# Kernel tuning notes

Hardware: AMD Instinct MI355X
Metric: run time of the kernel (lower is better)

## Reference

```python
import jax, jax.numpy as jnp
import numpy as np

HEADS = 16
D_MODEL = 1024
D_K = D_MODEL // HEADS


def setup_inputs() -> dict:
    key = jax.random.key(0)
    ks = jax.random.split(key, 11)
    B, S = 4, 2048
    scale = 1.0 / np.sqrt(D_MODEL)
    inp = {
        "query": jax.random.normal(ks[0], (B, S, D_MODEL), dtype=jnp.float32),
        "key": jax.random.normal(ks[1], (B, S, D_MODEL), dtype=jnp.float32),
        "value": jax.random.normal(ks[2], (B, S, D_MODEL), dtype=jnp.float32),
        "Wq": jax.random.normal(ks[3], (D_MODEL, D_MODEL), dtype=jnp.float32) * scale,
        "bq": jnp.zeros((D_MODEL,), dtype=jnp.float32),
        "Wk": jax.random.normal(ks[4], (D_MODEL, D_MODEL), dtype=jnp.float32) * scale,
        "bk": jnp.zeros((D_MODEL,), dtype=jnp.float32),
        "Wv": jax.random.normal(ks[5], (D_MODEL, D_MODEL), dtype=jnp.float32) * scale,
        "bv": jnp.zeros((D_MODEL,), dtype=jnp.float32),
        "Wo": jax.random.normal(ks[6], (D_MODEL, D_MODEL), dtype=jnp.float32) * scale,
        "bo": jnp.zeros((D_MODEL,), dtype=jnp.float32),
    }
    return inp


def reference(query, key, value, Wq, bq, Wk, bk, Wv, bv, Wo, bo):
    B, S, _ = query.shape
    # Linear projections, split into heads: [B,S,D] -> [B,H,S,d_k]
    def proj(x, W, b):
        y = x @ W.T + b
        return y.reshape(B, S, HEADS, D_K).transpose(0, 2, 1, 3)

    q = proj(query, Wq, bq)
    k = proj(key, Wk, bk)
    v = proj(value, Wv, bv)

    scores = jnp.einsum("bhqd,bhkd->bhqk", q, k) / jnp.sqrt(jnp.float32(D_K))
    p_attn = jax.nn.softmax(scores, axis=-1)  # dropout is identity in eval
    x = jnp.einsum("bhqk,bhkd->bhqd", p_attn, v)
    x = x.transpose(0, 2, 1, 3).reshape(B, S, HEADS * D_K)
    return x @ Wo.T + bo
```

## Files before the change

kernel.cpp:

```cpp
#include <hip/hip_runtime.h>
#include <hip/hip_bf16.h>
#include <stdint.h>

#define D_MODEL 1024
#define HEADS   16
#define DK      64
#define BATCH   4
#define SEQ     2048
#define MROWS   (BATCH * SEQ)

typedef __attribute__((ext_vector_type(8))) short bf16x8;
typedef __attribute__((ext_vector_type(4))) float f32x4;
typedef __attribute__((ext_vector_type(16))) float f32x16;
typedef __attribute__((ext_vector_type(4))) unsigned int u32x4;
typedef __attribute__((ext_vector_type(2))) unsigned int u32x2;

#define SCQ 0.18033688011112042f

__device__ __forceinline__ unsigned pk2bf(float a, float b) {
  __hip_bfloat162 h = __float22bfloat162_rn(float2{a, b});
  union { __hip_bfloat162 h; unsigned u; } c; c.h = h;
  return c.u;
}
__device__ __forceinline__ unsigned short n2bf(float f) {
  __hip_bfloat16 h = __float2bfloat16(f);
  union { __hip_bfloat16 h; unsigned short s; } c; c.h = h;
  return c.s;
}

__device__ __forceinline__ void gl_lds16(const void* g, void* l) {
  __builtin_amdgcn_global_load_lds(
      (const __attribute__((address_space(1))) unsigned int*)g,
      (__attribute__((address_space(3))) unsigned int*)l, 16, 0, 0);
}

__global__ __launch_bounds__(256) void cvt4(const float* __restrict__ w0, const float* __restrict__ w1,
                                            const float* __restrict__ w2, const float* __restrict__ w3,
                                            unsigned short* __restrict__ o0, unsigned short* __restrict__ o1,
                                            unsigned short* __restrict__ o2, unsigned short* __restrict__ o3) {
  const int which = blockIdx.x >> 10;
  const float* in; unsigned short* out;
  if (which == 0)      { in = w0; out = o0; }
  else if (which == 1) { in = w1; out = o1; }
  else if (which == 2) { in = w2; out = o2; }
  else                 { in = w3; out = o3; }
  const int i = ((blockIdx.x & 1023) * 256 + threadIdx.x) * 4;
  f32x4 v = *(const f32x4*)(in + i);
  u32x2 w;
  w[0] = pk2bf(v[0], v[1]);
  w[1] = pk2bf(v[2], v[3]);
  *(u32x2*)(out + i) = w;
}

__global__ __launch_bounds__(256) void qkv_gemm(const float* __restrict__ Aq, const float* __restrict__ Ak,
                                                const float* __restrict__ Av,
                                                const unsigned short* __restrict__ Bq,
                                                const unsigned short* __restrict__ Bk,
                                                const unsigned short* __restrict__ Bv,
                                                const float* __restrict__ bq_, const float* __restrict__ bk_,
                                                const float* __restrict__ bv_,
                                                unsigned short* __restrict__ Qo, unsigned short* __restrict__ Ko,
                                                unsigned short* __restrict__ Vo) {
  __shared__ unsigned short As[2][128 * 40];
  __shared__ unsigned short Bs[2][128 * 40];

  const int which = blockIdx.x >> 9;
  const int bx = blockIdx.x & 511;
  const float* Af = which == 0 ? Aq : which == 1 ? Ak : Av;
  const unsigned short* Bw = which == 0 ? Bq : which == 1 ? Bk : Bv;
  const float* bias = which == 0 ? bq_ : which == 1 ? bk_ : bv_;

  const int tid = threadIdx.x;
  const int lane = tid & 63, wid = tid >> 6;
  const int l16 = lane & 15, lg = lane >> 4;
  const int wrow = (wid >> 1) * 64, wcol = (wid & 1) * 64;

  const int swzb = (bx & 7) * 64 + (bx >> 3);
  const int m0 = (swzb >> 3) * 128, n0 = (swzb & 7) * 128;

  const int sr2 = tid >> 1, sc16 = (tid & 1) * 16;
  const float* aSrc = Af + (size_t)(m0 + sr2) * D_MODEL + sc16;
  const unsigned short* bSrc = Bw + (size_t)(n0 + sr2) * D_MODEL + sc16;

  f32x4 acc[4][4];
  const f32x4 zero = {0.f, 0.f, 0.f, 0.f};
#pragma unroll
  for (int i = 0; i < 4; ++i)
#pragma unroll
    for (int j = 0; j < 4; ++j) acc[i][j] = zero;

  f32x4 a0 = *(const f32x4*)aSrc, a1 = *(const f32x4*)(aSrc + 4),
        a2 = *(const f32x4*)(aSrc + 8), a3 = *(const f32x4*)(aSrc + 12);
  u32x4 br0 = *(const u32x4*)bSrc, br1 = *(const u32x4*)(bSrc + 8);

#pragma unroll 1
  for (int kt = 0; kt < D_MODEL / 32; ++kt) {
    const int buf = kt & 1;
    u32x4 pa, pb;
    pa[0] = pk2bf(a0[0], a0[1]); pa[1] = pk2bf(a0[2], a0[3]);
    pa[2] = pk2bf(a1[0], a1[1]); pa[3] = pk2bf(a1[2], a1[3]);
    pb[0] = pk2bf(a2[0], a2[1]); pb[1] = pk2bf(a2[2], a2[3]);
    pb[2] = pk2bf(a3[0], a3[1]); pb[3] = pk2bf(a3[2], a3[3]);
    *(u32x4*)&As[buf][sr2 * 40 + sc16] = pa;
    *(u32x4*)&As[buf][sr2 * 40 + sc16 + 8] = pb;
    *(u32x4*)&Bs[buf][sr2 * 40 + sc16] = br0;
    *(u32x4*)&Bs[buf][sr2 * 40 + sc16 + 8] = br1;
    __syncthreads();
    if (kt + 1 < D_MODEL / 32) {
      const float* an = aSrc + (kt + 1) * 32;
      a0 = *(const f32x4*)an; a1 = *(const f32x4*)(an + 4);
      a2 = *(const f32x4*)(an + 8); a3 = *(const f32x4*)(an + 12);
      const unsigned short* bn = bSrc + (kt + 1) * 32;
      br0 = *(const u32x4*)bn; br1 = *(const u32x4*)(bn + 8);
    }

    bf16x8 af[4], bfr[4];
#pragma unroll
    for (int i = 0; i < 4; ++i) {
      af[i]  = *(const bf16x8*)&As[buf][(wrow + i * 16 + l16) * 40 + lg * 8];
      bfr[i] = *(const bf16x8*)&Bs[buf][(wcol + i * 16 + l16) * 40 + lg * 8];
    }
#pragma unroll
    for (int i = 0; i < 4; ++i)
#pragma unroll
      for (int j = 0; j < 4; ++j)
        acc[i][j] = __builtin_amdgcn_mfma_f32_16x16x32_bf16(af[i], bfr[j], acc[i][j], 0, 0, 0);
  }

  const float scale = (which == 0) ? SCQ : 1.0f;
#pragma unroll
  for (int j = 0; j < 4; ++j) {
    const int col = n0 + wcol + j * 16 + l16;
    const float bv = bias[col];
    if (which == 2) {
      const int hh = col >> 6, dd = col & 63;
#pragma unroll
      for (int i = 0; i < 4; ++i) {
        const int row0 = m0 + wrow + i * 16 + lg * 4;
        u32x2 pw;
        pw[0] = pk2bf(acc[i][j][0] + bv, acc[i][j][1] + bv);
        pw[1] = pk2bf(acc[i][j][2] + bv, acc[i][j][3] + bv);
        unsigned short* dst = Vo +
            ((((size_t)(row0 >> 11) * HEADS + hh) * DK + dd) * SEQ + (row0 & (SEQ - 1)));
        *(u32x2*)dst = pw;
      }
    } else {
      unsigned short* Outp = which == 0 ? Qo : Ko;
#pragma unroll
      for (int i = 0; i < 4; ++i) {
        const int row0 = m0 + wrow + i * 16 + lg * 4;
#pragma unroll
        for (int r = 0; r < 4; ++r)
          Outp[(size_t)(row0 + r) * D_MODEL + col] = n2bf((acc[i][j][r] + bv) * scale);
      }
    }
  }
}

__global__ __launch_bounds__(256) void out_gemm(const unsigned short* __restrict__ Ab,
                                                const unsigned short* __restrict__ Bw,
                                                const float* __restrict__ bias,
                                                float* __restrict__ Outp) {
  __shared__ unsigned short As[2][128 * 40];
  __shared__ unsigned short Bs[2][128 * 40];

  const int tid = threadIdx.x;
  const int lane = tid & 63, wid = tid >> 6;
  const int l16 = lane & 15, lg = lane >> 4;
  const int wrow = (wid >> 1) * 64, wcol = (wid & 1) * 64;

  const int bx = blockIdx.x;
  const int swzb = (bx & 7) * 64 + (bx >> 3);
  const int m0 = (swzb >> 3) * 128, n0 = (swzb & 7) * 128;

  const int sr2 = tid >> 1, sc16 = (tid & 1) * 16;
  const unsigned short* aSrc = Ab + (size_t)(m0 + sr2) * D_MODEL + sc16;
  const unsigned short* bSrc = Bw + (size_t)(n0 + sr2) * D_MODEL + sc16;

  f32x4 acc[4][4];
  const f32x4 zero = {0.f, 0.f, 0.f, 0.f};
#pragma unroll
  for (int i = 0; i < 4; ++i)
#pragma unroll
    for (int j = 0; j < 4; ++j) acc[i][j] = zero;

  u32x4 ar0 = *(const u32x4*)aSrc, ar1 = *(const u32x4*)(aSrc + 8);
  u32x4 br0 = *(const u32x4*)bSrc, br1 = *(const u32x4*)(bSrc + 8);

#pragma unroll 1
  for (int kt = 0; kt < D_MODEL / 32; ++kt) {
    const int buf = kt & 1;
    *(u32x4*)&As[buf][sr2 * 40 + sc16] = ar0;
    *(u32x4*)&As[buf][sr2 * 40 + sc16 + 8] = ar1;
    *(u32x4*)&Bs[buf][sr2 * 40 + sc16] = br0;
    *(u32x4*)&Bs[buf][sr2 * 40 + sc16 + 8] = br1;
    __syncthreads();
    if (kt + 1 < D_MODEL / 32) {
      const unsigned short* an = aSrc + (kt + 1) * 32;
      ar0 = *(const u32x4*)an; ar1 = *(const u32x4*)(an + 8);
      const unsigned short* bn = bSrc + (kt + 1) * 32;
      br0 = *(const u32x4*)bn; br1 = *(const u32x4*)(bn + 8);
    }

    bf16x8 af[4], bfr[4];
#pragma unroll
    for (int i = 0; i < 4; ++i) {
      af[i]  = *(const bf16x8*)&As[buf][(wrow + i * 16 + l16) * 40 + lg * 8];
      bfr[i] = *(const bf16x8*)&Bs[buf][(wcol + i * 16 + l16) * 40 + lg * 8];
    }
#pragma unroll
    for (int i = 0; i < 4; ++i)
#pragma unroll
      for (int j = 0; j < 4; ++j)
        acc[i][j] = __builtin_amdgcn_mfma_f32_16x16x32_bf16(af[i], bfr[j], acc[i][j], 0, 0, 0);
  }

#pragma unroll
  for (int j = 0; j < 4; ++j) {
    const int col = n0 + wcol + j * 16 + l16;
    const float bv = bias[col];
#pragma unroll
    for (int i = 0; i < 4; ++i) {
      const int row0 = m0 + wrow + i * 16 + lg * 4;
#pragma unroll
      for (int r = 0; r < 4; ++r)
        Outp[(size_t)(row0 + r) * D_MODEL + col] = acc[i][j][r] + bv;
    }
  }
}

__global__ __launch_bounds__(256, 4) void attn_v11(const unsigned short* __restrict__ Qb,
                                                   const unsigned short* __restrict__ Kb,
                                                   const unsigned short* __restrict__ Vtg,
                                                   unsigned short* __restrict__ Xo) {
  __shared__ unsigned short Ks[2][32 * 128];
  __shared__ unsigned short Vt[2][32 * 128];
  __shared__ float Lbuf[4][32];

  const int tid = threadIdx.x;
  const int lane = tid & 63, w = tid >> 6;
  const int l32 = lane & 31, hi = lane >> 5;
  const int rsel = l32 >> 1;
  const int xorm = rsel << 3;
  const int cbase = (l32 & 1) * 64 + hi * 8;

  const int p = blockIdx.x;
  const int lb = (p & 7) * 128 + (p >> 3);
  const int qb = lb & 15, bh = lb >> 4;
  const int b = bh >> 4, h = bh & 15;

  const size_t srow0 = (size_t)b * SEQ + qb * 128;
  const unsigned short* Qp = Qb + srow0 * D_MODEL + h * DK;
  const unsigned short* Kp = Kb + (size_t)b * SEQ * D_MODEL + h * DK;
  const unsigned short* Vp = Vtg + (size_t)bh * DK * SEQ;

  bf16x8 qfrag[4];
#pragma unroll
  for (int s = 0; s < 4; ++s)
    qfrag[s] = *(const bf16x8*)(Qp + (size_t)(w * 32 + l32) * D_MODEL + s * 16 + hi * 8);

  const unsigned short* kSrc[2];
  const unsigned short* vSrc[2];
  int ldsByte[2];
#pragma unroll
  for (int c = 0; c < 2; ++c) {
    const int eo = (tid + c * 256) * 8;
    const int rp = eo >> 7;
    const int cl = (eo & 127) ^ ((rp & 15) << 3);
    const int tr = rp * 2 + (cl >> 6);
    const int cc = cl & 63;
    kSrc[c] = Kp + (size_t)tr * D_MODEL + cc;
    vSrc[c] = Vp + (size_t)tr * SEQ + cc;
    ldsByte[c] = (tid + c * 256) * 16;
  }

#pragma unroll
  for (int c = 0; c < 2; ++c) {
    gl_lds16(kSrc[c], (char*)Ks[0] + ldsByte[c]);
    gl_lds16(vSrc[c], (char*)Vt[0] + ldsByte[c]);
  }

  f32x16 acc[2];
#pragma unroll
  for (int i = 0; i < 16; ++i) { acc[0][i] = 0.f; acc[1][i] = 0.f; }
  float lsum = 0.f;

#pragma unroll 1
  for (int kb = 0; kb < SEQ / 64; ++kb) {
    const int buf = kb & 1;
    __syncthreads();
    if (kb + 1 < SEQ / 64) {
#pragma unroll
      for (int c = 0; c < 2; ++c) {
        gl_lds16(kSrc[c] + (size_t)(kb + 1) * 64 * D_MODEL, (char*)Ks[buf ^ 1] + ldsByte[c]);
        gl_lds16(vSrc[c] + (size_t)(kb + 1) * 64, (char*)Vt[buf ^ 1] + ldsByte[c]);
      }
    }

#pragma unroll
    for (int tt = 0; tt < 2; ++tt) {
      f32x16 d;
#pragma unroll
      for (int i = 0; i < 16; ++i) d[i] = 0.f;
#pragma unroll
      for (int s = 0; s < 4; ++s) {
        bf16x8 kf = *(const bf16x8*)&Ks[buf][(tt * 16 + rsel) * 128 + ((cbase + s * 16) ^ xorm)];
        d = __builtin_amdgcn_mfma_f32_32x32x16_bf16(kf, qfrag[s], d, 0, 0, 0);
      }

      unsigned pk[4][2];
#pragma unroll
      for (int g = 0; g < 4; ++g) {
        const float e0 = __builtin_amdgcn_exp2f(d[g * 4 + 0]);
        const float e1 = __builtin_amdgcn_exp2f(d[g * 4 + 1]);
        const float e2 = __builtin_amdgcn_exp2f(d[g * 4 + 2]);
        const float e3 = __builtin_amdgcn_exp2f(d[g * 4 + 3]);
        lsum += (e0 + e1) + (e2 + e3);
        pk[g][0] = pk2bf(e0, e1);
        pk[g][1] = pk2bf(e2, e3);
      }

#pragma unroll
      for (int s2 = 0; s2 < 2; ++s2) {
        unsigned a0 = pk[2 * s2][0], b0 = pk[2 * s2 + 1][0];
        unsigned a1 = pk[2 * s2][1], b1 = pk[2 * s2 + 1][1];
        asm("v_permlane32_swap_b32 %0, %1" : "+v"(a0), "+v"(b0));
        asm("v_permlane32_swap_b32 %0, %1" : "+v"(a1), "+v"(b1));
        union { unsigned u[4]; bf16x8 v; } pf;
        pf.u[0] = a0; pf.u[1] = a1; pf.u[2] = b0; pf.u[3] = b1;
        const int tcol = tt * 32 + s2 * 16;
#pragma unroll
        for (int dt = 0; dt < 2; ++dt) {
          bf16x8 vf = *(const bf16x8*)&Vt[buf][(dt * 16 + rsel) * 128 + ((cbase + tcol) ^ xorm)];
          acc[dt] = __builtin_amdgcn_mfma_f32_32x32x16_bf16(pf.v, vf, acc[dt], 0, 0, 0);
        }
      }
    }
  }

  lsum += __shfl_xor(lsum, 32);
  if (hi == 0) Lbuf[w][l32] = lsum;

  unsigned short* dst = Xo + (srow0 + w * 32) * D_MODEL + h * DK;
#pragma unroll
  for (int reg = 0; reg < 16; ++reg) {
    const int q = (reg & 3) + 8 * (reg >> 2) + 4 * hi;
    const float inv = 1.f / Lbuf[w][q];
#pragma unroll
    for (int dt = 0; dt < 2; ++dt)
      dst[(size_t)q * D_MODEL + dt * 32 + l32] = n2bf(acc[dt][reg] * inv);
  }
}

extern "C" void kernel_launch(void* const* d_in, const int* in_sizes, int n_in,
                              void* d_out, int out_size, void* d_ws, size_t ws_size,
                              hipStream_t stream) {
  const float* query = (const float*)d_in[0];
  const float* key_  = (const float*)d_in[1];
  const float* value = (const float*)d_in[2];
  const float* Wq = (const float*)d_in[3];
  const float* bq = (const float*)d_in[4];
  const float* Wk = (const float*)d_in[5];
  const float* bk = (const float*)d_in[6];
  const float* Wv = (const float*)d_in[7];
  const float* bv = (const float*)d_in[8];
  const float* Wo = (const float*)d_in[9];
  const float* bo = (const float*)d_in[10];

  unsigned short* ws  = (unsigned short*)d_ws;
  unsigned short* WqB = ws;
  unsigned short* WkB = WqB + (1u << 20);
  unsigned short* WvB = WkB + (1u << 20);
  unsigned short* WoB = WvB + (1u << 20);
  unsigned short* Qb  = WoB + (1u << 20);
  unsigned short* Kb  = Qb + (size_t)MROWS * D_MODEL;
  unsigned short* Vtg = Kb + (size_t)MROWS * D_MODEL;
  unsigned short* Xb  = Vtg + (size_t)MROWS * D_MODEL;
  if (ws_size < (size_t)(4u * (1u << 20) + 4u * (size_t)MROWS * D_MODEL) * 2u) return;

  cvt4<<<4096, 256, 0, stream>>>(Wq, Wk, Wv, Wo, WqB, WkB, WvB, WoB);

  qkv_gemm<<<1536, 256, 0, stream>>>(query, key_, value, WqB, WkB, WvB, bq, bk, bv, Qb, Kb, Vtg);

  attn_v11<<<1024, 256, 0, stream>>>(Qb, Kb, Vtg, Xb);

  out_gemm<<<512, 256, 0, stream>>>(Xb, WoB, bo, (float*)d_out);
}
```

Measured before the change: 215.7 us.

## Process two query tiles per wave in attention to reuse K/V LDS fragments

Each attention block now covers 256 query rows instead of 128, with every wave holding two 32-row Q tiles. The K and V fragments read from LDS are reused across both tiles, halving LDS reads and global K/V traffic per query row. The grid shrinks from 1024 to 512 blocks and launch bounds drop to 2 blocks per SM. The trade-off is roughly double the accumulator and Q register use, lower occupancy, and fewer blocks to spread across CUs.

```diff
diff --git a/kernel.cpp b/kernel.cpp
--- a/kernel.cpp
+++ b/kernel.cpp
@@ -229,13 +229,13 @@
   }
 }
 
-__global__ __launch_bounds__(256, 4) void attn_v11(const unsigned short* __restrict__ Qb,
+__global__ __launch_bounds__(256, 2) void attn_v12(const unsigned short* __restrict__ Qb,
                                                    const unsigned short* __restrict__ Kb,
                                                    const unsigned short* __restrict__ Vtg,
                                                    unsigned short* __restrict__ Xo) {
   __shared__ unsigned short Ks[2][32 * 128];
   __shared__ unsigned short Vt[2][32 * 128];
-  __shared__ float Lbuf[4][32];
+  __shared__ float Lbuf[4][64];
 
   const int tid = threadIdx.x;
   const int lane = tid & 63, w = tid >> 6;
@@ -245,19 +245,21 @@
   const int cbase = (l32 & 1) * 64 + hi * 8;
 
   const int p = blockIdx.x;
-  const int lb = (p & 7) * 128 + (p >> 3);
-  const int qb = lb & 15, bh = lb >> 4;
+  const int lb = (p & 7) * 64 + (p >> 3);
+  const int qb = lb & 7, bh = lb >> 3;
   const int b = bh >> 4, h = bh & 15;
 
-  const size_t srow0 = (size_t)b * SEQ + qb * 128;
+  const size_t srow0 = (size_t)b * SEQ + qb * 256;
   const unsigned short* Qp = Qb + srow0 * D_MODEL + h * DK;
   const unsigned short* Kp = Kb + (size_t)b * SEQ * D_MODEL + h * DK;
   const unsigned short* Vp = Vtg + (size_t)bh * DK * SEQ;
 
-  bf16x8 qfrag[4];
-#pragma unroll
-  for (int s = 0; s < 4; ++s)
-    qfrag[s] = *(const bf16x8*)(Qp + (size_t)(w * 32 + l32) * D_MODEL + s * 16 + hi * 8);
+  bf16x8 qfrag[2][4];
+#pragma unroll
+  for (int qt = 0; qt < 2; ++qt)
+#pragma unroll
+    for (int s = 0; s < 4; ++s)
+      qfrag[qt][s] = *(const bf16x8*)(Qp + (size_t)(w * 64 + qt * 32 + l32) * D_MODEL + s * 16 + hi * 8);
 
   const unsigned short* kSrc[2];
   const unsigned short* vSrc[2];
@@ -280,10 +282,12 @@
     gl_lds16(vSrc[c], (char*)Vt[0] + ldsByte[c]);
   }
 
-  f32x16 acc[2];
-#pragma unroll
-  for (int i = 0; i < 16; ++i) { acc[0][i] = 0.f; acc[1][i] = 0.f; }
-  float lsum = 0.f;
+  f32x16 acc[2][2];
+#pragma unroll
+  for (int i = 0; i < 16; ++i) {
+    acc[0][0][i] = 0.f; acc[0][1][i] = 0.f; acc[1][0][i] = 0.f; acc[1][1][i] = 0.f;
+  }
+  float lsum[2] = {0.f, 0.f};
 
 #pragma unroll 1
   for (int kb = 0; kb < SEQ / 64; ++kb) {
@@ -299,57 +303,75 @@
 
 #pragma unroll
     for (int tt = 0; tt < 2; ++tt) {
-      f32x16 d;
-#pragma unroll
-      for (int i = 0; i < 16; ++i) d[i] = 0.f;
-#pragma unroll
-      for (int s = 0; s < 4; ++s) {
-        bf16x8 kf = *(const bf16x8*)&Ks[buf][(tt * 16 + rsel) * 128 + ((cbase + s * 16) ^ xorm)];
-        d = __builtin_amdgcn_mfma_f32_32x32x16_bf16(kf, qfrag[s], d, 0, 0, 0);
+      bf16x8 kf[4];
+#pragma unroll
+      for (int s = 0; s < 4; ++s)
+        kf[s] = *(const bf16x8*)&Ks[buf][(tt * 16 + rsel) * 128 + ((cbase + s * 16) ^ xorm)];
+
+      unsigned pk[2][4][2];
+#pragma unroll
+      for (int qt = 0; qt < 2; ++qt) {
+        f32x16 d;
+#pragma unroll
+        for (int i = 0; i < 16; ++i) d[i] = 0.f;
+#pragma unroll
+        for (int s = 0; s < 4; ++s)
+          d = __builtin_amdgcn_mfma_f32_32x32x16_bf16(kf[s], qfrag[qt][s], d, 0, 0, 0);
+
+#pragma unroll
+        for (int g = 0; g < 4; ++g) {
+          const float e0 = __builtin_amdgcn_exp2f(d[g * 4 + 0]);
+          const float e1 = __builtin_amdgcn_exp2f(d[g * 4 + 1]);
+          const float e2 = __builtin_amdgcn_exp2f(d[g * 4 + 2]);
+          const float e3 = __builtin_amdgcn_exp2f(d[g * 4 + 3]);
+          lsum[qt] += (e0 + e1) + (e2 + e3);
+          pk[qt][g][0] = pk2bf(e0, e1);
+          pk[qt][g][1] = pk2bf(e2, e3);
+        }
       }
 
-      unsigned pk[4][2];
-#pragma unroll
-      for (int g = 0; g < 4; ++g) {
-        const float e0 = __builtin_amdgcn_exp2f(d[g * 4 + 0]);
-        const float e1 = __builtin_amdgcn_exp2f(d[g * 4 + 1]);
-        const float e2 = __builtin_amdgcn_exp2f(d[g * 4 + 2]);
-        const float e3 = __builtin_amdgcn_exp2f(d[g * 4 + 3]);
-        lsum += (e0 + e1) + (e2 + e3);
-        pk[g][0] = pk2bf(e0, e1);
-        pk[g][1] = pk2bf(e2, e3);
-      }
-
 #pragma unroll
       for (int s2 = 0; s2 < 2; ++s2) {
-        unsigned a0 = pk[2 * s2][0], b0 = pk[2 * s2 + 1][0];
-        unsigned a1 = pk[2 * s2][1], b1 = pk[2 * s2 + 1][1];
-        asm("v_permlane32_swap_b32 %0, %1" : "+v"(a0), "+v"(b0));
-        asm("v_permlane32_swap_b32 %0, %1" : "+v"(a1), "+v"(b1));
-        union { unsigned u[4]; bf16x8 v; } pf;
-        pf.u[0] = a0; pf.u[1] = a1; pf.u[2] = b0; pf.u[3] = b1;
+        bf16x8 pfv[2];
+#pragma unroll
+        for (int qt = 0; qt < 2; ++qt) {
+          unsigned a0 = pk[qt][2 * s2][0], b0 = pk[qt][2 * s2 + 1][0];
+          unsigned a1 = pk[qt][2 * s2][1], b1 = pk[qt][2 * s2 + 1][1];
+          asm("v_permlane32_swap_b32 %0, %1" : "+v"(a0), "+v"(b0));
+          asm("v_permlane32_swap_b32 %0, %1" : "+v"(a1), "+v"(b1));
+          union { unsigned u[4]; bf16x8 v; } pf;
+          pf.u[0] = a0; pf.u[1] = a1; pf.u[2] = b0; pf.u[3] = b1;
+          pfv[qt] = pf.v;
+        }
         const int tcol = tt * 32 + s2 * 16;
 #pragma unroll
         for (int dt = 0; dt < 2; ++dt) {
           bf16x8 vf = *(const bf16x8*)&Vt[buf][(dt * 16 + rsel) * 128 + ((cbase + tcol) ^ xorm)];
-          acc[dt] = __builtin_amdgcn_mfma_f32_32x32x16_bf16(pf.v, vf, acc[dt], 0, 0, 0);
+#pragma unroll
+          for (int qt = 0; qt < 2; ++qt)
+            acc[qt][dt] = __builtin_amdgcn_mfma_f32_32x32x16_bf16(pfv[qt], vf, acc[qt][dt], 0, 0, 0);
         }
       }
     }
   }
 
-  lsum += __shfl_xor(lsum, 32);
-  if (hi == 0) Lbuf[w][l32] = lsum;
-
-  unsigned short* dst = Xo + (srow0 + w * 32) * D_MODEL + h * DK;
-#pragma unroll
-  for (int reg = 0; reg < 16; ++reg) {
-    const int q = (reg & 3) + 8 * (reg >> 2) + 4 * hi;
-    const float inv = 1.f / Lbuf[w][q];
-#pragma unroll
-    for (int dt = 0; dt < 2; ++dt)
-      dst[(size_t)q * D_MODEL + dt * 32 + l32] = n2bf(acc[dt][reg] * inv);
-  }
+#pragma unroll
+  for (int qt = 0; qt < 2; ++qt) {
+    lsum[qt] += __shfl_xor(lsum[qt], 32);
+    if (hi == 0) Lbuf[w][qt * 32 + l32] = lsum[qt];
+  }
+
+  unsigned short* dst = Xo + (srow0 + w * 64) * D_MODEL + h * DK;
+#pragma unroll
+  for (int qt = 0; qt < 2; ++qt)
+#pragma unroll
+    for (int reg = 0; reg < 16; ++reg) {
+      const int q = qt * 32 + (reg & 3) + 8 * (reg >> 2) + 4 * hi;
+      const float inv = 1.f / Lbuf[w][q];
+#pragma unroll
+      for (int dt = 0; dt < 2; ++dt)
+        dst[(size_t)q * D_MODEL + dt * 32 + l32] = n2bf(acc[qt][dt][reg] * inv);
+    }
 }
 
 extern "C" void kernel_launch(void* const* d_in, const int* in_sizes, int n_in,
@@ -382,7 +404,7 @@
 
   qkv_gemm<<<1536, 256, 0, stream>>>(query, key_, value, WqB, WkB, WvB, bq, bk, bv, Qb, Kb, Vtg);
 
-  attn_v11<<<1024, 256, 0, stream>>>(Qb, Kb, Vtg, Xb);
+  attn_v12<<<512, 256, 0, stream>>>(Qb, Kb, Vtg, Xb);
 
   out_gemm<<<512, 256, 0, stream>>>(Xb, WoB, bo, (float*)d_out);
 }
```

New measurement: 203.4 us, median of 3. 5.7% less time.
